# Kernel optimization log

Hardware: AMD Instinct MI355X
Metric: run time of the kernel (lower is better)

## Reference

```python
import jax, jax.numpy as jnp
import numpy as np

G, FO, FI = 8, 64, 64   # n_group, fo, fi
N_ITER = 3
B, H, W = 32, 64, 64


def setup_inputs() -> dict:
    key = jax.random.key(0)
    k1, k2, k3 = jax.random.split(key, 3)
    x = jax.random.normal(k1, (B, G * FI, H, W), jnp.float32)
    # kaiming_normal on [fo*g, fi, 1, 1] -> std = sqrt(2/fi); stored as [g, fo, fi]
    weight = jax.random.normal(k2, (G, FO, FI), jnp.float32) * np.float32(np.sqrt(2.0 / FI))
    bias = jax.random.normal(k3, (FO,), jnp.float32)
    return {"x": x, "weight": weight, "bias": bias}


def reference(x, weight, bias):
    b, c, h, w = x.shape
    g, fo, fi = weight.shape
    # grouped 1x1 conv: split channels into g groups of fi, contract each with its [fo, fi] block
    xr = x.reshape(b, g, fi, h, w)
    con = jnp.einsum('bgihw,goi->bgohw', xr, weight)  # [B, g, fo, H, W]
    beta = jnp.zeros((1, g, 1, 1, 1), dtype=x.dtype)
    for i in range(N_ITER):
        alpha = jax.nn.sigmoid(beta)
        v = jnp.sum(alpha * con, axis=1, keepdims=True)      # [B, 1, fo, H, W]
        if i == N_ITER - 1:
            return v[:, 0] + bias[None, :, None, None]       # [B, fo, H, W]
        beta = beta + jnp.sum(v * con, axis=2, keepdims=True)  # [B, g, 1, H, W]
```

## Files before the change

### kernel.cpp

```cpp
#include <hip/hip_runtime.h>


#define NG 8
#define NFO 64
#define NFI 64
#define NB 32
#define NH 64
#define NW 64
#define HW (NH * NW)

typedef float v2f __attribute__((ext_vector_type(2)));

__device__ __forceinline__ void stage_piece(const float* gsrc, float* ldst) {
    __builtin_amdgcn_global_load_lds(
        (const __attribute__((address_space(1))) void*)gsrc,
        (__attribute__((address_space(3))) void*)ldst, 16, 0, 0);
}

__global__ __launch_bounds__(256) void dynrout_kernel(
    const float* __restrict__ x, const float* __restrict__ weight,
    const float* __restrict__ bias, float* __restrict__ out)
{
    const int tid = threadIdx.x;
    const int p = tid & 63;
    const int q = __builtin_amdgcn_readfirstlane(tid >> 6);

    const int wg = blockIdx.x;
    const int b = wg >> 6;
    const int h = wg & 63;

    __shared__ __align__(16) float smem[4096];

    const float* xrow = x + (size_t)b * (NG * NFI) * HW + (size_t)h * NW;
    const float* gpiece = xrow + (size_t)(p >> 4) * HW + (size_t)(p & 15) * 4;

    float con[8][16];
#pragma unroll
    for (int g = 0; g < 8; ++g)
#pragma unroll
        for (int f = 0; f < 16; ++f) con[g][f] = 0.f;

    {
        float* dst = smem;
        const float* g0 = gpiece;
        stage_piece(g0 + (size_t)(q * 8) * HW,       dst + (q * 2) * 256);
        stage_piece(g0 + (size_t)(q * 8 + 4) * HW,   dst + (q * 2 + 1) * 256);
    }
    __syncthreads();

#pragma unroll
    for (int c = 0; c < 16; ++c) {
        if (c < 15) {
            float* dst = smem + ((c + 1) & 1) * 2048;
            const float* g0 = gpiece + (size_t)((c + 1) * 32) * HW;
            stage_piece(g0 + (size_t)(q * 8) * HW,     dst + (q * 2) * 256);
            stage_piece(g0 + (size_t)(q * 8 + 4) * HW, dst + (q * 2 + 1) * 256);
        }

        const int g = c >> 1;
        const float* bufp = smem + (c & 1) * 2048;

        v2f xp[16];
#pragma unroll
        for (int jp = 0; jp < 16; ++jp) {
            xp[jp].x = bufp[(2 * jp) * 64 + p];
            xp[jp].y = bufp[(2 * jp + 1) * 64 + p];
        }

        const float* wq = weight + ((size_t)g * NFO + (size_t)q * 16) * NFI + (c & 1) * 32;
#pragma unroll
        for (int f = 0; f < 16; ++f) {
            const float* wr = wq + (size_t)f * NFI;
            v2f a0 = {0.f, 0.f}, a1 = {0.f, 0.f};
#pragma unroll
            for (int jp = 0; jp < 16; jp += 2) {
                const v2f w0 = *(const v2f*)(wr + 2 * jp);
                const v2f w1 = *(const v2f*)(wr + 2 * jp + 2);
                a0 = __builtin_elementwise_fma(w0, xp[jp], a0);
                a1 = __builtin_elementwise_fma(w1, xp[jp + 1], a1);
            }
            con[g][f] += (a0.x + a1.x) + (a0.y + a1.y);
        }
        __syncthreads();
    }

    float* pbuf   = smem;
    float* alphaS = smem + 2048;
    float* betaS  = smem + 2560;

    float v[16];

#pragma unroll
    for (int f = 0; f < 16; ++f) {
        float s = con[0][f];
#pragma unroll
        for (int g = 1; g < 8; ++g) s += con[g][f];
        v[f] = 0.5f * s;
    }
#pragma unroll
    for (int g = 0; g < 8; ++g) {
        float s = 0.f;
#pragma unroll
        for (int f = 0; f < 16; ++f) s = fmaf(v[f], con[g][f], s);
        pbuf[(q * 8 + g) * 64 + p] = s;
    }
    __syncthreads();
    for (int k = tid; k < 512; k += 256) {
        const int gg = k >> 6, pp = k & 63;
        const float bs = pbuf[gg * 64 + pp] + pbuf[512 + gg * 64 + pp] +
                         pbuf[1024 + gg * 64 + pp] + pbuf[1536 + gg * 64 + pp];
        betaS[gg * 64 + pp] = bs;
        alphaS[gg * 64 + pp] = 1.f / (1.f + __expf(-bs));
    }
    __syncthreads();

    float a[8];
#pragma unroll
    for (int g = 0; g < 8; ++g) a[g] = alphaS[g * 64 + p];
#pragma unroll
    for (int f = 0; f < 16; ++f) {
        float s = 0.f;
#pragma unroll
        for (int g = 0; g < 8; ++g) s = fmaf(a[g], con[g][f], s);
        v[f] = s;
    }
#pragma unroll
    for (int g = 0; g < 8; ++g) {
        float s = 0.f;
#pragma unroll
        for (int f = 0; f < 16; ++f) s = fmaf(v[f], con[g][f], s);
        pbuf[(q * 8 + g) * 64 + p] = s;
    }
    __syncthreads();
    for (int k = tid; k < 512; k += 256) {
        const int gg = k >> 6, pp = k & 63;
        const float bs = betaS[gg * 64 + pp] +
                         pbuf[gg * 64 + pp] + pbuf[512 + gg * 64 + pp] +
                         pbuf[1024 + gg * 64 + pp] + pbuf[1536 + gg * 64 + pp];
        alphaS[gg * 64 + pp] = 1.f / (1.f + __expf(-bs));
    }
    __syncthreads();

#pragma unroll
    for (int g = 0; g < 8; ++g) a[g] = alphaS[g * 64 + p];

    const float* bq = bias + q * 16;
    float* orow = out + (((size_t)b * NFO + (size_t)q * 16) * NH + h) * NW + p;
#pragma unroll
    for (int f = 0; f < 16; ++f) {
        float s = bq[f];
#pragma unroll
        for (int g = 0; g < 8; ++g) s = fmaf(a[g], con[g][f], s);
        orow[(size_t)f * HW] = s;
    }
}

extern "C" void kernel_launch(void* const* d_in, const int* in_sizes, int n_in,
                              void* d_out, int out_size, void* d_ws, size_t ws_size,
                              hipStream_t stream) {
    const float* x      = (const float*)d_in[0];
    const float* weight = (const float*)d_in[1];
    const float* bias   = (const float*)d_in[2];
    float* out = (float*)d_out;

    dynrout_kernel<<<dim3(NB * NH), dim3(256), 0, stream>>>(x, weight, bias, out);
}
```

Measured before the change: 561.3 us.

## Use 512-thread blocks with triple-buffered per-group staging and 8 outputs per thread

Doubles the block to 512 threads (8 waves), so each thread owns 8 output channels instead of 16, halving the con register array. Each stage now loads a full group of 64 input channels into one of three LDS buffers, and explicit vmcnt waits plus raw barriers replace the old two-buffer scheme with __syncthreads. The inner loop is reordered so each x pair read from LDS is reused across 8 weight rows. The aim is lower register pressure and more latency hiding through deeper prefetch, at the cost of 48 KB of LDS per block, which may limit how many blocks fit per CU.

```diff
diff --git a/kernel.cpp b/kernel.cpp
--- a/kernel.cpp
+++ b/kernel.cpp
@@ -17,7 +17,7 @@
         (__attribute__((address_space(3))) void*)ldst, 16, 0, 0);
 }
 
-__global__ __launch_bounds__(256) void dynrout_kernel(
+__global__ __launch_bounds__(512) void dynrout_kernel(
     const float* __restrict__ x, const float* __restrict__ weight,
     const float* __restrict__ bias, float* __restrict__ out)
 {
@@ -29,69 +29,64 @@
     const int b = wg >> 6;
     const int h = wg & 63;
 
-    __shared__ __align__(16) float smem[4096];
+    __shared__ __align__(16) float smem[12288];
 
     const float* xrow = x + (size_t)b * (NG * NFI) * HW + (size_t)h * NW;
-    const float* gpiece = xrow + (size_t)(p >> 4) * HW + (size_t)(p & 15) * 4;
+    const float* gsrc0 = xrow + ((size_t)(q * 8 + (p >> 4))) * HW + (size_t)(p & 15) * 4;
+    const int ldst0 = q * 8 * 64;
 
-    float con[8][16];
-#pragma unroll
-    for (int g = 0; g < 8; ++g)
-#pragma unroll
-        for (int f = 0; f < 16; ++f) con[g][f] = 0.f;
-
-    {
-        float* dst = smem;
-        const float* g0 = gpiece;
-        stage_piece(g0 + (size_t)(q * 8) * HW,       dst + (q * 2) * 256);
-        stage_piece(g0 + (size_t)(q * 8 + 4) * HW,   dst + (q * 2 + 1) * 256);
-    }
-    __syncthreads();
+    float con[8][8];
 
 #pragma unroll
-    for (int c = 0; c < 16; ++c) {
-        if (c < 15) {
-            float* dst = smem + ((c + 1) & 1) * 2048;
-            const float* g0 = gpiece + (size_t)((c + 1) * 32) * HW;
-            stage_piece(g0 + (size_t)(q * 8) * HW,     dst + (q * 2) * 256);
-            stage_piece(g0 + (size_t)(q * 8 + 4) * HW, dst + (q * 2 + 1) * 256);
+    for (int g = 0; g < 2; ++g) {
+        const float* s0 = gsrc0 + (size_t)(g * 64) * HW;
+        float* dst = smem + g * 4096 + ldst0;
+        stage_piece(s0, dst);
+        stage_piece(s0 + 4 * HW, dst + 256);
+    }
+
+#pragma unroll
+    for (int c = 0; c < 8; ++c) {
+        if (c < 7) asm volatile("s_waitcnt vmcnt(2)" ::: "memory");
+        else       asm volatile("s_waitcnt vmcnt(0)" ::: "memory");
+        __builtin_amdgcn_s_barrier();
+
+        if (c < 6) {
+            const float* s0 = gsrc0 + (size_t)((c + 2) * 64) * HW;
+            float* dst = smem + ((c + 2) % 3) * 4096 + ldst0;
+            stage_piece(s0, dst);
+            stage_piece(s0 + 4 * HW, dst + 256);
         }
 
-        const int g = c >> 1;
-        const float* bufp = smem + (c & 1) * 2048;
+        const float* buf = smem + (c % 3) * 4096;
+        const float* wrow = weight + ((size_t)(c * 64 + q * 8)) * 64;
 
-        v2f xp[16];
+        v2f acc[8];
 #pragma unroll
-        for (int jp = 0; jp < 16; ++jp) {
-            xp[jp].x = bufp[(2 * jp) * 64 + p];
-            xp[jp].y = bufp[(2 * jp + 1) * 64 + p];
+        for (int f = 0; f < 8; ++f) acc[f] = (v2f){0.f, 0.f};
+#pragma unroll
+        for (int jp = 0; jp < 32; ++jp) {
+            v2f xv;
+            xv.x = buf[(2 * jp) * 64 + p];
+            xv.y = buf[(2 * jp + 1) * 64 + p];
+#pragma unroll
+            for (int f = 0; f < 8; ++f) {
+                const v2f wv = *(const v2f*)(wrow + f * 64 + 2 * jp);
+                acc[f] = __builtin_elementwise_fma(wv, xv, acc[f]);
+            }
         }
-
-        const float* wq = weight + ((size_t)g * NFO + (size_t)q * 16) * NFI + (c & 1) * 32;
 #pragma unroll
-        for (int f = 0; f < 16; ++f) {
-            const float* wr = wq + (size_t)f * NFI;
-            v2f a0 = {0.f, 0.f}, a1 = {0.f, 0.f};
-#pragma unroll
-            for (int jp = 0; jp < 16; jp += 2) {
-                const v2f w0 = *(const v2f*)(wr + 2 * jp);
-                const v2f w1 = *(const v2f*)(wr + 2 * jp + 2);
-                a0 = __builtin_elementwise_fma(w0, xp[jp], a0);
-                a1 = __builtin_elementwise_fma(w1, xp[jp + 1], a1);
-            }
-            con[g][f] += (a0.x + a1.x) + (a0.y + a1.y);
-        }
-        __syncthreads();
+        for (int f = 0; f < 8; ++f) con[c][f] = acc[f].x + acc[f].y;
     }
 
     float* pbuf   = smem;
-    float* alphaS = smem + 2048;
-    float* betaS  = smem + 2560;
+    float* alphaS = smem + 4096;
+    float* betaS  = smem + 4608;
 
-    float v[16];
+    float v[8];
 
 #pragma unroll
-    for (int f = 0; f < 16; ++f) {
+    for (int f = 0; f < 8; ++f) {
         float s = con[0][f];
 #pragma unroll
         for (int g = 1; g < 8; ++g) s += con[g][f];
@@ -101,14 +96,15 @@
     for (int g = 0; g < 8; ++g) {
         float s = 0.f;
 #pragma unroll
-        for (int f = 0; f < 16; ++f) s = fmaf(v[f], con[g][f], s);
+        for (int f = 0; f < 8; ++f) s = fmaf(v[f], con[g][f], s);
         pbuf[(q * 8 + g) * 64 + p] = s;
     }
     __syncthreads();
-    for (int k = tid; k < 512; k += 256) {
-        const int gg = k >> 6, pp = k & 63;
-        const float bs = pbuf[gg * 64 + pp] + pbuf[512 + gg * 64 + pp] +
-                         pbuf[1024 + gg * 64 + pp] + pbuf[1536 + gg * 64 + pp];
+    {
+        const int gg = tid >> 6, pp = tid & 63;
+        float bs = 0.f;
+#pragma unroll
+        for (int w = 0; w < 8; ++w) bs += pbuf[(w * 8 + gg) * 64 + pp];
         betaS[gg * 64 + pp] = bs;
         alphaS[gg * 64 + pp] = 1.f / (1.f + __expf(-bs));
     }
@@ -118,7 +114,7 @@
 #pragma unroll
     for (int g = 0; g < 8; ++g) a[g] = alphaS[g * 64 + p];
 #pragma unroll
-    for (int f = 0; f < 16; ++f) {
+    for (int f = 0; f < 8; ++f) {
         float s = 0.f;
 #pragma unroll
         for (int g = 0; g < 8; ++g) s = fmaf(a[g], con[g][f], s);
@@ -128,15 +124,15 @@
     for (int g = 0; g < 8; ++g) {
         float s = 0.f;
 #pragma unroll
-        for (int f = 0; f < 16; ++f) s = fmaf(v[f], con[g][f], s);
+        for (int f = 0; f < 8; ++f) s = fmaf(v[f], con[g][f], s);
         pbuf[(q * 8 + g) * 64 + p] = s;
     }
     __syncthreads();
-    for (int k = tid; k < 512; k += 256) {
-        const int gg = k >> 6, pp = k & 63;
-        const float bs = betaS[gg * 64 + pp] +
-                         pbuf[gg * 64 + pp] + pbuf[512 + gg * 64 + pp] +
-                         pbuf[1024 + gg * 64 + pp] + pbuf[1536 + gg * 64 + pp];
+    {
+        const int gg = tid >> 6, pp = tid & 63;
+        float bs = betaS[gg * 64 + pp];
+#pragma unroll
+        for (int w = 0; w < 8; ++w) bs += pbuf[(w * 8 + gg) * 64 + pp];
         alphaS[gg * 64 + pp] = 1.f / (1.f + __expf(-bs));
     }
     __syncthreads();
@@ -144,10 +140,10 @@
 #pragma unroll
     for (int g = 0; g < 8; ++g) a[g] = alphaS[g * 64 + p];
 
-    const float* bq = bias + q * 16;
-    float* orow = out + (((size_t)b * NFO + (size_t)q * 16) * NH + h) * NW + p;
+    const float* bq = bias + q * 8;
+    float* orow = out + (((size_t)b * NFO + (size_t)q * 8) * NH + h) * NW + p;
 #pragma unroll
-    for (int f = 0; f < 16; ++f) {
+    for (int f = 0; f < 8; ++f) {
         float s = bq[f];
 #pragma unroll
         for (int g = 0; g < 8; ++g) s = fmaf(a[g], con[g][f], s);
@@ -163,5 +159,5 @@
     const float* bias   = (const float*)d_in[2];
     float* out = (float*)d_out;
 
-    dynrout_kernel<<<dim3(NB * NH), dim3(256), 0, stream>>>(x, weight, bias, out);
+    dynrout_kernel<<<dim3(NB * NH), dim3(512), 0, stream>>>(x, weight, bias, out);
 }
```

Measured after the change: 1.224 ms. +118.0%, slower.
